# Kernel optimization log

Measured on AMD Instinct MI355X. Metric: run time of the kernel, lower is better.

The kernel has to match this reference:

```python
import jax, jax.numpy as jnp
import numpy as np

C, T, H = 256, 16, 8
D = C // H  # head dim = 32
SCALE = float((D * T) ** 0.5)


def setup_inputs() -> dict:
    key = jax.random.key(0)
    kx, kk, kq, kv = jax.random.split(key, 4)
    B, P = 8, 1024
    x = jax.random.normal(kx, (B, C, P, T), dtype=jnp.float32)
    # 1x1 conv weights, no bias -> [out_ch, in_ch]
    Wk = jax.random.normal(kk, (C, C), dtype=jnp.float32) * 0.02
    Wq = jax.random.normal(kq, (C, C), dtype=jnp.float32) * 0.02
    Wv = jax.random.normal(kv, (C, C), dtype=jnp.float32) * 0.02
    return {"x": x, "Wk": Wk, "Wq": Wq, "Wv": Wv}


def _proj_split(W, x):
    # 1x1 conv == channel matmul, then split heads: b (h d) p t -> b h d p t
    B, _, P, Tt = x.shape
    y = jnp.einsum('oc,bcpt->bopt', W, x)
    return y.reshape(B, H, D, P, Tt)


def reference(x, Wk, Wq, Wv):
    B, _, P, Tt = x.shape
    k = _proj_split(Wk, x)  # [B,H,D,P,T]
    q = _proj_split(Wq, x)
    v = _proj_split(Wv, x)
    # energy over spatial positions, contracting head-dim and time
    energy = jnp.einsum('bhdpt,bhdqt->bhpq', k, q)  # [B,H,P,P]
    attn = jax.nn.softmax(energy / SCALE, axis=-1)
    out = jnp.einsum('bhpq,bhdpt->bhdqt', attn, v)  # [B,H,D,P,T]
    return out.reshape(B, C, P, Tt)
```

## Files before the change

### kernel.cpp

```cpp
#include <hip/hip_runtime.h>


typedef unsigned short u16;
typedef unsigned int u32;
typedef unsigned long long u64;
typedef __attribute__((ext_vector_type(8))) short bfx8;
typedef __attribute__((ext_vector_type(4))) float fx4;

constexpr float KC1 = 1.4426950408889634f / 22.627416997969522f;

__device__ __forceinline__ u16 f2bf(float f) {
  u32 u = __builtin_bit_cast(u32, f);
  return (u16)((u + 0x7fffu + ((u >> 16) & 1u)) >> 16);
}
__device__ __forceinline__ float bf2f(u16 v) {
  return __builtin_bit_cast(float, (u32)v << 16);
}
__device__ __forceinline__ fx4 mfma16(bfx8 a, bfx8 b, fx4 c) {
  return __builtin_amdgcn_mfma_f32_16x16x32_bf16(a, b, c, 0, 0, 0);
}
typedef __attribute__((address_space(1))) const unsigned int* as1p;
typedef __attribute__((address_space(3))) unsigned int* as3p;
__device__ __forceinline__ void gll16(const void* g, void* l) {
  __builtin_amdgcn_global_load_lds((as1p)g, (as3p)l, 16, 0, 0);
}
__device__ __forceinline__ void midbar_() { __builtin_amdgcn_s_barrier(); }
__device__ __forceinline__ void pend_() {
  __builtin_amdgcn_s_barrier();
  __builtin_amdgcn_sched_barrier(0);
}
#define VMC4 do { asm volatile("s_waitcnt vmcnt(4)" ::: "memory"); \
                  __builtin_amdgcn_sched_barrier(0); } while (0)
#define VMC0 do { asm volatile("s_waitcnt vmcnt(0)" ::: "memory"); \
                  __builtin_amdgcn_sched_barrier(0); } while (0)

template <bool SWAP, int NT, int LK>
__device__ __forceinline__ void gemm8(const u16* __restrict__ Ag,
                                      const u16* __restrict__ Bg,
                                      u16* lds, fx4 (&acc)[2][4][2][2],
                                      int wv, int lane) {
  const int l15 = lane & 15, kg = lane >> 4, l7 = lane & 7;
  const int wr = wv >> 2, wn = wv & 3;
  const int rsub = lane >> 3, csub = (lane & 7) * 8;
  constexpr int A0 = 0, A1 = 16384, B0 = 32768, B1 = 49152;
  bfx8 af[4][2], bf[2][2][2];

  auto stg = [&](const u16* g, int ldsoff, int tile, int half) {
    const u16* gp = g + (size_t)(half * 128 + wv * 16 + rsub) * LK + tile * 64 + csub;
    u16* lp = lds + ldsoff + half * 8192 + wv * 1024;
    gll16(gp, lp);
    gll16(gp + (size_t)8 * LK, lp + 512);
  };
  auto LA = [&](int boff, int mh) {
    const u16* base = lds + boff + mh * 8192 + wr * 4096;
#pragma unroll
    for (int mt = 0; mt < 4; ++mt)
#pragma unroll
      for (int kk = 0; kk < 2; ++kk)
        af[mt][kk] = *(const bfx8*)(base + (mt * 16 + l15) * 64 + (((kk << 2) + kg) ^ l7) * 8);
  };
  auto LB = [&](int boff, int nh) {
    const u16* base = lds + boff + nh * 8192 + wn * 2048;
#pragma unroll
    for (int nt = 0; nt < 2; ++nt)
#pragma unroll
      for (int kk = 0; kk < 2; ++kk)
        bf[nh][nt][kk] = *(const bfx8*)(base + (nt * 16 + l15) * 64 + (((kk << 2) + kg) ^ l7) * 8);
  };
  auto MM = [&](int mh, int nh) {
    __builtin_amdgcn_s_setprio(1);
#pragma unroll
    for (int mt = 0; mt < 4; ++mt)
#pragma unroll
      for (int nt = 0; nt < 2; ++nt)
#pragma unroll
        for (int kk = 0; kk < 2; ++kk) {
          if constexpr (SWAP)
            acc[mh][mt][nh][nt] = mfma16(bf[nh][nt][kk], af[mt][kk], acc[mh][mt][nh][nt]);
          else
            acc[mh][mt][nh][nt] = mfma16(af[mt][kk], bf[nh][nt][kk], acc[mh][mt][nh][nt]);
        }
    __builtin_amdgcn_s_setprio(0);
  };

  stg(Ag, A0, 0, 0); stg(Ag, A0, 0, 1);
  stg(Bg, B0, 0, 0); stg(Bg, B0, 0, 1);
  stg(Ag, A1, 1, 0); stg(Bg, B1, 1, 1);
  VMC4;
  pend_();

  constexpr int NI = NT / 2;
#pragma unroll 1
  for (int i = 0; i < NI; ++i) {
    const int t = 2 * i;
    const bool more = (i + 1 < NI);
    LA(A0, 0); LB(B0, 0);
    stg(Ag, A1, t + 1, 1);
    midbar_(); MM(0, 0); pend_();
    LB(B0, 1);
    stg(Bg, B1, t + 1, 0);
    midbar_(); MM(0, 1); pend_();
    LA(A0, 1);
    if (more) stg(Ag, A0, t + 2, 0);
    midbar_(); MM(1, 1); pend_();
    if (more) stg(Bg, B0, t + 2, 1);
    midbar_(); MM(1, 0);
    if (more) { VMC4; } else { VMC0; }
    pend_();
    LA(A1, 0); LB(B1, 0);
    if (more) stg(Ag, A0, t + 2, 1);
    midbar_(); MM(0, 0); pend_();
    LB(B1, 1);
    if (more) stg(Bg, B0, t + 2, 0);
    midbar_(); MM(0, 1); pend_();
    LA(A1, 1);
    if (more) stg(Ag, A1, t + 3, 0);
    midbar_(); MM(1, 1); pend_();
    if (more) stg(Bg, B1, t + 3, 1);
    midbar_(); MM(1, 0);
    if (more) { VMC4; }
    pend_();
  }
}

__global__ __launch_bounds__(256) void k_wconv(const float* __restrict__ Wk,
                                               const float* __restrict__ Wq,
                                               const float* __restrict__ Wv,
                                               u16* __restrict__ Wall) {
  int blk = blockIdx.x;
  int pr = blk >> 5;
  const float* src = (pr == 0) ? Wk : ((pr == 1) ? Wq : Wv);
  int oc = (blk & 31) * 8 + (threadIdx.x >> 5);
  int Cc = threadIdx.x & 31;
  const float4* s4 = (const float4*)(src + oc * 256 + Cc * 8);
  float4 a = s4[0], b = s4[1];
  alignas(16) u16 t[8] = {f2bf(a.x), f2bf(a.y), f2bf(a.z), f2bf(a.w),
                          f2bf(b.x), f2bf(b.y), f2bf(b.z), f2bf(b.w)};
  int o = pr * 256 + oc;
  int pos = (Cc & ~7) + ((Cc & 7) ^ (o & 7));
  *(uint4*)(Wall + o * 256 + pos * 8) = *(const uint4*)t;
}

__global__ __launch_bounds__(256) void k_xt(const float* __restrict__ x,
                                            u16* __restrict__ Xbf) {
  __shared__ u16 Xs[128 * 256];
  int b = blockIdx.x >> 7;
  int n0 = (blockIdx.x & 127) * 128;
  int tid = threadIdx.x;
  int ng = tid & 31, cgrp = tid >> 5;
  const float* xb = x + (size_t)b * 4194304 + n0 + ng * 4;
#pragma unroll
  for (int it = 0; it < 4; ++it) {
    int Cc = cgrp + it * 8;
    float4 v[8];
#pragma unroll
    for (int i = 0; i < 8; ++i)
      v[i] = *(const float4*)(xb + (size_t)(Cc * 8 + i) * 16384);
#pragma unroll
    for (int j = 0; j < 4; ++j) {
      int n = ng * 4 + j;
      alignas(16) u16 c8v[8];
#pragma unroll
      for (int i = 0; i < 8; ++i) c8v[i] = f2bf(((const float*)&v[i])[j]);
      int pos = (Cc & ~7) + ((Cc & 7) ^ (n & 7));
      *(uint4*)&Xs[n * 256 + pos * 8] = *(const uint4*)c8v;
    }
  }
  __syncthreads();
  u16* xo = Xbf + (size_t)b * 4194304 + (size_t)n0 * 256;
#pragma unroll
  for (int it = 0; it < 16; ++it) {
    int idx = tid + it * 256;
    int n = idx >> 5, chp = idx & 31;
    uint4 v = *(const uint4*)&Xs[n * 256 + chp * 8];
    *(uint4*)&xo[(size_t)n * 256 + chp * 8] = v;
  }
}

__global__ __launch_bounds__(512) void k_proj2(const u16* __restrict__ Xbf,
                                               const u16* __restrict__ Wall,
                                               u16* __restrict__ Kb, u16* __restrict__ Qb,
                                               u16* __restrict__ Vb) {
  __shared__ u16 lds[65536];
  int bid = blockIdx.x;
  int vid = (bid & 7) * 192 + (bid >> 3);
  int nidx = vid / 3;
  int otile = vid - nidx * 3;
  int b = nidx >> 6, ntile = nidx & 63;
  int tid = threadIdx.x, lane = tid & 63, wv = tid >> 6;
  int l15 = lane & 15, kg = lane >> 4;
  int wr = wv >> 2, wn = wv & 3;
  const u16* Ag = Wall + otile * 65536;
  const u16* Bg = Xbf + (size_t)b * 4194304 + (size_t)ntile * 65536;
  fx4 acc[2][4][2][2];
#pragma unroll
  for (int mh = 0; mh < 2; ++mh)
#pragma unroll
    for (int mt = 0; mt < 4; ++mt)
#pragma unroll
      for (int nh = 0; nh < 2; ++nh)
#pragma unroll
        for (int nt = 0; nt < 2; ++nt) acc[mh][mt][nh][nt] = (fx4)0.0f;

  gemm8<true, 4, 256>(Ag, Bg, lds, acc, wv, lane);

  u16* dst = (otile == 0) ? Kb : ((otile == 1) ? Qb : Vb);
#pragma unroll
  for (int mh = 0; mh < 2; ++mh)
#pragma unroll
    for (int mt = 0; mt < 4; ++mt) {
      int o = mh * 128 + wr * 64 + mt * 16 + l15;
      int h = o >> 5;
      int d = o & 31;
      size_t bhro = (size_t)(b * 8 + h) * 524288;
      int f0 = d * 16 + kg * 4;
      int f7 = f0 & 7;
      int fc = f0 >> 3;
#pragma unroll
      for (int nh = 0; nh < 2; ++nh)
#pragma unroll
        for (int nt = 0; nt < 2; ++nt) {
          int p = ntile * 16 + nh * 8 + wn * 2 + nt;
          alignas(8) u16 e4[4];
#pragma unroll
          for (int j = 0; j < 4; ++j) e4[j] = f2bf(acc[mh][mt][nh][nt][j]);
          int ch = fc ^ (p & 7);
          *(u64*)(dst + bhro + (size_t)p * 512 + ch * 8 + f7) = *(const u64*)e4;
        }
    }
}

__global__ __launch_bounds__(512) void k_egemm(const u16* __restrict__ Qb,
                                               const u16* __restrict__ Kb,
                                               u16* __restrict__ Pt,
                                               float* __restrict__ Zpart) {
  __shared__ u16 lds[65536];
  int bid = blockIdx.x;
  int vid = (bid & 7) * 128 + (bid >> 3);
  int bh = vid >> 4, qt = (vid >> 2) & 3, pt = vid & 3;
  int q0 = qt * 256, p0 = pt * 256;
  int tid = threadIdx.x, lane = tid & 63, wv = tid >> 6;
  int l15 = lane & 15, kg = lane >> 4;
  int wr = wv >> 2, wn = wv & 3;
  const u16* Ag = Qb + (size_t)bh * 524288 + (size_t)q0 * 512;
  const u16* Bg = Kb + (size_t)bh * 524288 + (size_t)p0 * 512;
  fx4 acc[2][4][2][2];
#pragma unroll
  for (int mh = 0; mh < 2; ++mh)
#pragma unroll
    for (int mt = 0; mt < 4; ++mt)
#pragma unroll
      for (int nh = 0; nh < 2; ++nh)
#pragma unroll
        for (int nt = 0; nt < 2; ++nt) acc[mh][mt][nh][nt] = (fx4)0.0f;

  gemm8<true, 8, 512>(Ag, Bg, lds, acc, wv, lane);

  size_t pbase = (size_t)bh * 1048576;
  float zac[2][2][4];
#pragma unroll
  for (int nh = 0; nh < 2; ++nh)
#pragma unroll
    for (int nt = 0; nt < 2; ++nt)
#pragma unroll
      for (int j = 0; j < 4; ++j) zac[nh][nt][j] = 0.f;
#pragma unroll
  for (int mh = 0; mh < 2; ++mh)
#pragma unroll
    for (int mt = 0; mt < 4; ++mt) {
      int q = q0 + mh * 128 + wr * 64 + mt * 16 + l15;
      size_t qrow = pbase + (size_t)q * 1024;
      int q7 = l15 & 7;
#pragma unroll
      for (int nh = 0; nh < 2; ++nh)
#pragma unroll
        for (int nt = 0; nt < 2; ++nt) {
          int p4 = p0 + nh * 128 + wn * 32 + nt * 16 + kg * 4;
          alignas(8) u16 e4[4];
#pragma unroll
          for (int j = 0; j < 4; ++j) {
            float e = exp2f(acc[mh][mt][nh][nt][j] * KC1);
            zac[nh][nt][j] += e;
            e4[j] = f2bf(e);
          }
          int ch = (p4 >> 3) ^ q7;
          *(u64*)(Pt + qrow + ch * 8 + (p4 & 7)) = *(const u64*)e4;
        }
    }
#pragma unroll
  for (int nh = 0; nh < 2; ++nh)
#pragma unroll
    for (int nt = 0; nt < 2; ++nt)
#pragma unroll
      for (int j = 0; j < 4; ++j) {
        float v = zac[nh][nt][j];
        v += __shfl_xor(v, 1);
        v += __shfl_xor(v, 2);
        v += __shfl_xor(v, 4);
        v += __shfl_xor(v, 8);
        zac[nh][nt][j] = v;
      }
  if (l15 == 0) {
    size_t zb = (size_t)(qt * 2 + wr) * 65536 + (size_t)bh * 1024;
#pragma unroll
    for (int nh = 0; nh < 2; ++nh)
#pragma unroll
      for (int nt = 0; nt < 2; ++nt) {
        int p4 = p0 + nh * 128 + wn * 32 + nt * 16 + kg * 4;
        float4 zv;
        zv.x = zac[nh][nt][0]; zv.y = zac[nh][nt][1];
        zv.z = zac[nh][nt][2]; zv.w = zac[nh][nt][3];
        *(float4*)&Zpart[zb + p4] = zv;
      }
  }
}

__global__ __launch_bounds__(256) void k_zfinal(const float* __restrict__ Zpart,
                                                float* __restrict__ RZ) {
  int idx = blockIdx.x * 256 + threadIdx.x;
  float s = 0.f;
#pragma unroll
  for (int k = 0; k < 8; ++k) s += Zpart[(size_t)k * 65536 + idx];
  RZ[idx] = 1.0f / s;
}

__global__ __launch_bounds__(256) void k_vt(const u16* __restrict__ Vb,
                                            const float* __restrict__ RZ,
                                            u16* __restrict__ Vt) {
  __shared__ u16 Vl[64 * 512];
  int bh = blockIdx.x >> 4;
  int ptile = blockIdx.x & 15;
  int tid = threadIdx.x;
  const u16* src = Vb + (size_t)bh * 524288 + (size_t)ptile * 32768;
#pragma unroll
  for (int it = 0; it < 16; ++it) {
    int idx = tid + it * 256;
    int pl = idx >> 6, g = idx & 63;
    float rz = RZ[bh * 1024 + ptile * 64 + pl];
    uint4 v = *(const uint4*)&src[(size_t)pl * 512 + g * 8];
    int cf = g ^ (pl & 7);
    u32 w[4] = {v.x, v.y, v.z, v.w};
    alignas(16) u16 c8v[8];
#pragma unroll
    for (int i = 0; i < 4; ++i) {
      c8v[2 * i]     = f2bf(bf2f((u16)w[i]) * rz);
      c8v[2 * i + 1] = f2bf(bf2f((u16)(w[i] >> 16)) * rz);
    }
    *(uint4*)&Vl[pl * 512 + cf * 8] = *(const uint4*)c8v;
  }
  __syncthreads();
  u16* dst = Vt + (size_t)bh * 524288;
#pragma unroll
  for (int it = 0; it < 16; ++it) {
    int f = (tid & 63) + (it & 7) * 64;
    int pc = (tid >> 6) * 2 + (it >> 3);
    int base = pc * 8 * 512 + f;
    u32 x0 = (u32)Vl[base] | ((u32)Vl[base + 512] << 16);
    u32 x1 = (u32)Vl[base + 1024] | ((u32)Vl[base + 1536] << 16);
    u32 x2 = (u32)Vl[base + 2048] | ((u32)Vl[base + 2560] << 16);
    u32 x3 = (u32)Vl[base + 3072] | ((u32)Vl[base + 3584] << 16);
    uint4 pk; pk.x = x0; pk.y = x1; pk.z = x2; pk.w = x3;
    int col = ptile * 8 + (pc ^ (f & 7));
    *(uint4*)&dst[(size_t)f * 1024 + col * 8] = pk;
  }
}

__global__ __launch_bounds__(512) void k_pv(const u16* __restrict__ Pt,
                                            const u16* __restrict__ Vt,
                                            float* __restrict__ out) {
  __shared__ u16 lds[65536];
  int bid = blockIdx.x;
  int vid = (bid & 7) * 64 + (bid >> 3);
  int bh = vid >> 3, tile = vid & 7;
  int q0 = (tile >> 1) * 256, f0 = (tile & 1) * 256;
  int tid = threadIdx.x, lane = tid & 63, wv = tid >> 6;
  int l15 = lane & 15, kg = lane >> 4;
  int wr = wv >> 2, wn = wv & 3;
  const u16* Ag = Pt + (size_t)bh * 1048576 + (size_t)q0 * 1024;
  const u16* Bg = Vt + (size_t)bh * 524288 + (size_t)f0 * 1024;
  fx4 acc[2][4][2][2];
#pragma unroll
  for (int mh = 0; mh < 2; ++mh)
#pragma unroll
    for (int mt = 0; mt < 4; ++mt)
#pragma unroll
      for (int nh = 0; nh < 2; ++nh)
#pragma unroll
        for (int nt = 0; nt < 2; ++nt) acc[mh][mt][nh][nt] = (fx4)0.0f;

  gemm8<true, 16, 1024>(Ag, Bg, lds, acc, wv, lane);

#pragma unroll
  for (int mh = 0; mh < 2; ++mh)
#pragma unroll
    for (int mt = 0; mt < 4; ++mt) {
      int q = q0 + mh * 128 + wr * 64 + mt * 16 + l15;
#pragma unroll
      for (int nh = 0; nh < 2; ++nh)
#pragma unroll
        for (int nt = 0; nt < 2; ++nt) {
          int fb = f0 + nh * 128 + wn * 32 + nt * 16 + kg * 4;
          int d = fb >> 4, t0 = fb & 15;
          float4 v;
          v.x = acc[mh][mt][nh][nt][0];
          v.y = acc[mh][mt][nh][nt][1];
          v.z = acc[mh][mt][nh][nt][2];
          v.w = acc[mh][mt][nh][nt][3];
          *(float4*)&out[(size_t)(bh * 32 + d) * 16384 + (size_t)q * 16 + t0] = v;
        }
    }
}

extern "C" void kernel_launch(void* const* d_in, const int* in_sizes, int n_in,
                              void* d_out, int out_size, void* d_ws, size_t ws_size,
                              hipStream_t stream) {
  (void)in_sizes; (void)n_in; (void)out_size; (void)ws_size;
  const float* x  = (const float*)d_in[0];
  const float* Wk = (const float*)d_in[1];
  const float* Wq = (const float*)d_in[2];
  const float* Wv = (const float*)d_in[3];
  float* out = (float*)d_out;

  u16* Kb  = (u16*)d_ws;
  u16* Qb  = Kb + 33554432;
  u16* Vb  = Qb + 33554432;
  u16* Xbf = Vb + 33554432;
  u16* Pt  = Xbf;
  u16* Vt  = Qb;
  float* Zpart = (float*)(Kb + 167772160);
  float* RZ = Zpart + 524288;
  u16* Wall = (u16*)(RZ + 65536);

  k_wconv<<<96, 256, 0, stream>>>(Wk, Wq, Wv, Wall);
  k_xt<<<1024, 256, 0, stream>>>(x, Xbf);
  k_proj2<<<1536, 512, 0, stream>>>(Xbf, Wall, Kb, Qb, Vb);
  k_egemm<<<1024, 512, 0, stream>>>(Qb, Kb, Pt, Zpart);
  k_zfinal<<<256, 256, 0, stream>>>(Zpart, RZ);
  k_vt<<<1024, 256, 0, stream>>>(Vb, RZ, Vt);
  k_pv<<<512, 512, 0, stream>>>(Pt, Vt, out);
}
```

Measured before the change: 348.4 us.

## Store K and Q in FP8 and run the energy GEMM with FP8 MFMA

The projection kernel now writes K and Q as scaled FP8 (e4m3, scaled by 16) instead of bf16, and the energy GEMM uses a new FP8 GEMM routine built on the 16x16x32 fp8 MFMA, with the exp scale constant divided by 256 to undo the scaling. This halves the bytes loaded for Q and K in the energy stage and uses the faster FP8 matrix path. The workspace layout is reorganised so Vt no longer aliases Qb. It risks accuracy loss in the softmax logits from FP8 quantisation.

```diff
diff --git a/kernel.cpp b/kernel.cpp
--- a/kernel.cpp
+++ b/kernel.cpp
@@ -1,6 +1,7 @@
 #include <hip/hip_runtime.h>
 
 
+typedef unsigned char u8;
 typedef unsigned short u16;
 typedef unsigned int u32;
 typedef unsigned long long u64;
@@ -8,6 +9,8 @@
 typedef __attribute__((ext_vector_type(4))) float fx4;
 
 constexpr float KC1 = 1.4426950408889634f / 22.627416997969522f;
+constexpr float KC8 = KC1 / 256.0f;
+constexpr float S8 = 16.0f;
 
 __device__ __forceinline__ u16 f2bf(float f) {
   u32 u = __builtin_bit_cast(u32, f);
@@ -18,6 +21,9 @@
 }
 __device__ __forceinline__ fx4 mfma16(bfx8 a, bfx8 b, fx4 c) {
   return __builtin_amdgcn_mfma_f32_16x16x32_bf16(a, b, c, 0, 0, 0);
+}
+__device__ __forceinline__ fx4 mfma8(long a, long b, fx4 c) {
+  return __builtin_amdgcn_mfma_f32_16x16x32_fp8_fp8(a, b, c, 0, 0, 0);
 }
 typedef __attribute__((address_space(1))) const unsigned int* as1p;
 typedef __attribute__((address_space(3))) unsigned int* as3p;
@@ -29,10 +35,8 @@
   __builtin_amdgcn_s_barrier();
   __builtin_amdgcn_sched_barrier(0);
 }
-#define VMC4 do { asm volatile("s_waitcnt vmcnt(4)" ::: "memory"); \
-                  __builtin_amdgcn_sched_barrier(0); } while (0)
-#define VMC0 do { asm volatile("s_waitcnt vmcnt(0)" ::: "memory"); \
-                  __builtin_amdgcn_sched_barrier(0); } while (0)
+#define VMC(n) do { asm volatile("s_waitcnt vmcnt(" #n ")" ::: "memory"); \
+                    __builtin_amdgcn_sched_barrier(0); } while (0)
 
 template <bool SWAP, int NT, int LK>
 __device__ __forceinline__ void gemm8(const u16* __restrict__ Ag,
@@ -86,7 +90,7 @@
   stg(Ag, A0, 0, 0); stg(Ag, A0, 0, 1);
   stg(Bg, B0, 0, 0); stg(Bg, B0, 0, 1);
   stg(Ag, A1, 1, 0); stg(Bg, B1, 1, 1);
-  VMC4;
+  VMC(4);
   pend_();
 
   constexpr int NI = NT / 2;
@@ -105,7 +109,7 @@
     midbar_(); MM(1, 1); pend_();
     if (more) stg(Bg, B0, t + 2, 1);
     midbar_(); MM(1, 0);
-    if (more) { VMC4; } else { VMC0; }
+    if (more) { VMC(4); } else { VMC(0); }
     pend_();
     LA(A1, 0); LB(B1, 0);
     if (more) stg(Ag, A0, t + 2, 1);
@@ -118,7 +122,90 @@
     midbar_(); MM(1, 1); pend_();
     if (more) stg(Bg, B1, t + 3, 1);
     midbar_(); MM(1, 0);
-    if (more) { VMC4; }
+    if (more) { VMC(4); }
+    pend_();
+  }
+}
+
+template <int NT, int LK>
+__device__ __forceinline__ void gemm8f(const u8* __restrict__ Ag,
+                                       const u8* __restrict__ Bg,
+                                       u8* lds, fx4 (&acc)[2][4][2][2],
+                                       int wv, int lane) {
+  const int l15 = lane & 15, kg = lane >> 4, l7 = lane & 7;
+  const int wr = wv >> 2, wn = wv & 3;
+  const int rs4 = lane >> 2, c16 = (lane & 3) * 16;
+  constexpr int A0 = 0, A1 = 16384, B0 = 32768, B1 = 49152;
+  long af[4][2], bf[2][2][2];
+
+  auto stg = [&](const u8* g, int ldsoff, int tile, int half) {
+    const u8* gp = g + (size_t)(half * 128 + wv * 16 + rs4) * LK + tile * 64 + c16;
+    gll16(gp, lds + ldsoff + half * 8192 + wv * 1024);
+  };
+  auto LA = [&](int boff, int mh) {
+    const u8* base = lds + boff + mh * 8192 + wr * 4096;
+#pragma unroll
+    for (int mt = 0; mt < 4; ++mt)
+#pragma unroll
+      for (int kk = 0; kk < 2; ++kk)
+        af[mt][kk] = *(const long*)(base + (mt * 16 + l15) * 64 + ((((kk << 2) + kg) ^ l7) << 3));
+  };
+  auto LB = [&](int boff, int nh) {
+    const u8* base = lds + boff + nh * 8192 + wn * 2048;
+#pragma unroll
+    for (int nt = 0; nt < 2; ++nt)
+#pragma unroll
+      for (int kk = 0; kk < 2; ++kk)
+        bf[nh][nt][kk] = *(const long*)(base + (nt * 16 + l15) * 64 + ((((kk << 2) + kg) ^ l7) << 3));
+  };
+  auto MM = [&](int mh, int nh) {
+    __builtin_amdgcn_s_setprio(1);
+#pragma unroll
+    for (int mt = 0; mt < 4; ++mt)
+#pragma unroll
+      for (int nt = 0; nt < 2; ++nt)
+#pragma unroll
+        for (int kk = 0; kk < 2; ++kk)
+          acc[mh][mt][nh][nt] = mfma8(bf[nh][nt][kk], af[mt][kk], acc[mh][mt][nh][nt]);
+    __builtin_amdgcn_s_setprio(0);
+  };
+
+  stg(Ag, A0, 0, 0); stg(Ag, A0, 0, 1);
+  stg(Bg, B0, 0, 0); stg(Bg, B0, 0, 1);
+  stg(Ag, A1, 1, 0); stg(Bg, B1, 1, 1);
+  VMC(2);
+  pend_();
+
+  constexpr int NI = NT / 2;
+#pragma unroll 1
+  for (int i = 0; i < NI; ++i) {
+    const int t = 2 * i;
+    const bool more = (i + 1 < NI);
+    LA(A0, 0); LB(B0, 0);
+    stg(Ag, A1, t + 1, 1);
+    midbar_(); MM(0, 0); pend_();
+    LB(B0, 1);
+    stg(Bg, B1, t + 1, 0);
+    midbar_(); MM(0, 1); pend_();
+    LA(A0, 1);
+    if (more) stg(Ag, A0, t + 2, 0);
+    midbar_(); MM(1, 1); pend_();
+    if (more) stg(Bg, B0, t + 2, 1);
+    midbar_(); MM(1, 0);
+    if (more) { VMC(2); } else { VMC(0); }
+    pend_();
+    LA(A1, 0); LB(B1, 0);
+    if (more) stg(Ag, A0, t + 2, 1);
+    midbar_(); MM(0, 0); pend_();
+    LB(B1, 1);
+    if (more) stg(Bg, B0, t + 2, 0);
+    midbar_(); MM(0, 1); pend_();
+    LA(A1, 1);
+    if (more) stg(Ag, A1, t + 3, 0);
+    midbar_(); MM(1, 1); pend_();
+    if (more) stg(Bg, B1, t + 3, 1);
+    midbar_(); MM(1, 0);
+    if (more) { VMC(2); }
     pend_();
   }
 }
@@ -179,7 +266,7 @@
 
 __global__ __launch_bounds__(512) void k_proj2(const u16* __restrict__ Xbf,
                                                const u16* __restrict__ Wall,
-                                               u16* __restrict__ Kb, u16* __restrict__ Qb,
+                                               u8* __restrict__ Kb8, u8* __restrict__ Qb8,
                                                u16* __restrict__ Vb) {
   __shared__ u16 lds[65536];
   int bid = blockIdx.x;
@@ -204,7 +291,6 @@
 
   gemm8<true, 4, 256>(Ag, Bg, lds, acc, wv, lane);
 
-  u16* dst = (otile == 0) ? Kb : ((otile == 1) ? Qb : Vb);
 #pragma unroll
   for (int mh = 0; mh < 2; ++mh)
 #pragma unroll
@@ -212,29 +298,45 @@
       int o = mh * 128 + wr * 64 + mt * 16 + l15;
       int h = o >> 5;
       int d = o & 31;
-      size_t bhro = (size_t)(b * 8 + h) * 524288;
       int f0 = d * 16 + kg * 4;
-      int f7 = f0 & 7;
-      int fc = f0 >> 3;
-#pragma unroll
-      for (int nh = 0; nh < 2; ++nh)
-#pragma unroll
-        for (int nt = 0; nt < 2; ++nt) {
-          int p = ntile * 16 + nh * 8 + wn * 2 + nt;
-          alignas(8) u16 e4[4];
-#pragma unroll
-          for (int j = 0; j < 4; ++j) e4[j] = f2bf(acc[mh][mt][nh][nt][j]);
-          int ch = fc ^ (p & 7);
-          *(u64*)(dst + bhro + (size_t)p * 512 + ch * 8 + f7) = *(const u64*)e4;
-        }
+      if (otile < 2) {
+        u8* dst = (otile == 0) ? Kb8 : Qb8;
+        size_t bhro = (size_t)(b * 8 + h) * 524288;
+        int fu = f0 >> 3, flo = f0 & 7;
+#pragma unroll
+        for (int nh = 0; nh < 2; ++nh)
+#pragma unroll
+          for (int nt = 0; nt < 2; ++nt) {
+            int p = ntile * 16 + nh * 8 + wn * 2 + nt;
+            const fx4& a4 = acc[mh][mt][nh][nt];
+            u32 w = __builtin_amdgcn_cvt_pk_fp8_f32(a4[0] * S8, a4[1] * S8, 0, false);
+            w = __builtin_amdgcn_cvt_pk_fp8_f32(a4[2] * S8, a4[3] * S8, w, true);
+            *(u32*)(dst + bhro + (size_t)p * 512 + ((fu ^ (p & 7)) << 3) + flo) = w;
+          }
+      } else {
+        size_t bhro = (size_t)(b * 8 + h) * 524288;
+        int f7 = f0 & 7;
+        int fc = f0 >> 3;
+#pragma unroll
+        for (int nh = 0; nh < 2; ++nh)
+#pragma unroll
+          for (int nt = 0; nt < 2; ++nt) {
+            int p = ntile * 16 + nh * 8 + wn * 2 + nt;
+            alignas(8) u16 e4[4];
+#pragma unroll
+            for (int j = 0; j < 4; ++j) e4[j] = f2bf(acc[mh][mt][nh][nt][j]);
+            int ch = fc ^ (p & 7);
+            *(u64*)(Vb + bhro + (size_t)p * 512 + ch * 8 + f7) = *(const u64*)e4;
+          }
+      }
     }
 }
 
-__global__ __launch_bounds__(512) void k_egemm(const u16* __restrict__ Qb,
-                                               const u16* __restrict__ Kb,
+__global__ __launch_bounds__(512) void k_egemm(const u8* __restrict__ Qb8,
+                                               const u8* __restrict__ Kb8,
                                                u16* __restrict__ Pt,
                                                float* __restrict__ Zpart) {
-  __shared__ u16 lds[65536];
+  __shared__ u8 lds[65536];
   int bid = blockIdx.x;
   int vid = (bid & 7) * 128 + (bid >> 3);
   int bh = vid >> 4, qt = (vid >> 2) & 3, pt = vid & 3;
@@ -242,8 +344,8 @@
   int tid = threadIdx.x, lane = tid & 63, wv = tid >> 6;
   int l15 = lane & 15, kg = lane >> 4;
   int wr = wv >> 2, wn = wv & 3;
-  const u16* Ag = Qb + (size_t)bh * 524288 + (size_t)q0 * 512;
-  const u16* Bg = Kb + (size_t)bh * 524288 + (size_t)p0 * 512;
+  const u8* Ag = Qb8 + (size_t)bh * 524288 + (size_t)q0 * 512;
+  const u8* Bg = Kb8 + (size_t)bh * 524288 + (size_t)p0 * 512;
   fx4 acc[2][4][2][2];
 #pragma unroll
   for (int mh = 0; mh < 2; ++mh)
@@ -254,7 +356,7 @@
 #pragma unroll
         for (int nt = 0; nt < 2; ++nt) acc[mh][mt][nh][nt] = (fx4)0.0f;
 
-  gemm8<true, 8, 512>(Ag, Bg, lds, acc, wv, lane);
+  gemm8f<8, 512>(Ag, Bg, lds, acc, wv, lane);
 
   size_t pbase = (size_t)bh * 1048576;
   float zac[2][2][4];
@@ -279,7 +381,7 @@
           alignas(8) u16 e4[4];
 #pragma unroll
           for (int j = 0; j < 4; ++j) {
-            float e = exp2f(acc[mh][mt][nh][nt][j] * KC1);
+            float e = exp2f(acc[mh][mt][nh][nt][j] * KC8);
             zac[nh][nt][j] += e;
             e4[j] = f2bf(e);
           }
@@ -421,20 +523,21 @@
   const float* Wv = (const float*)d_in[3];
   float* out = (float*)d_out;
 
-  u16* Kb  = (u16*)d_ws;
-  u16* Qb  = Kb + 33554432;
-  u16* Vb  = Qb + 33554432;
-  u16* Xbf = Vb + 33554432;
+  u8* base = (u8*)d_ws;
+  u8*  Kb8 = base;
+  u8*  Qb8 = base + 33554432;
+  u16* Vb  = (u16*)(base + 67108864);
+  u16* Xbf = (u16*)(base + 134217728);
   u16* Pt  = Xbf;
-  u16* Vt  = Qb;
-  float* Zpart = (float*)(Kb + 167772160);
+  u16* Vt  = (u16*)(base + 268435456);
+  float* Zpart = (float*)(base + 335544320);
   float* RZ = Zpart + 524288;
   u16* Wall = (u16*)(RZ + 65536);
 
   k_wconv<<<96, 256, 0, stream>>>(Wk, Wq, Wv, Wall);
   k_xt<<<1024, 256, 0, stream>>>(x, Xbf);
-  k_proj2<<<1536, 512, 0, stream>>>(Xbf, Wall, Kb, Qb, Vb);
-  k_egemm<<<1024, 512, 0, stream>>>(Qb, Kb, Pt, Zpart);
+  k_proj2<<<1536, 512, 0, stream>>>(Xbf, Wall, Kb8, Qb8, Vb);
+  k_egemm<<<1024, 512, 0, stream>>>(Qb8, Kb8, Pt, Zpart);
   k_zfinal<<<256, 256, 0, stream>>>(Zpart, RZ);
   k_vt<<<1024, 256, 0, stream>>>(Vb, RZ, Vt);
   k_pv<<<512, 512, 0, stream>>>(Pt, Vt, out);
```

Measured after the change: 320.8 us. 1.09x faster.
